# Performance work log

Hardware: AMD Instinct MI355X
Metric: run time of the kernel (lower is better)

The kernel has to match this reference:

```python
import jax, jax.numpy as jnp
import numpy as np

N, E, F_IN, H, D, C = 50000, 800000, 128, 4, 64, 40
HD = H * D
NEG_SLOPE = 0.2


def setup_inputs() -> dict:
    key = jax.random.key(0)
    ks = jax.random.split(key, 16)
    x = jax.random.normal(ks[0], (N, F_IN), dtype=jnp.float32)
    edge_index = jax.random.randint(ks[1], (2, E), 0, N, dtype=jnp.int64)
    def glorot(k, shape):
        fan = shape[0] + shape[-1]
        return jax.random.normal(k, shape, dtype=jnp.float32) * jnp.sqrt(2.0 / fan)
    params = {
        'W1': glorot(ks[2], (F_IN, HD)), 'as1': glorot(ks[3], (H, D)), 'ad1': glorot(ks[4], (H, D)), 'b1': jnp.zeros((HD,), jnp.float32),
        'W2': glorot(ks[5], (HD, HD)),   'as2': glorot(ks[6], (H, D)), 'ad2': glorot(ks[7], (H, D)), 'b2': jnp.zeros((HD,), jnp.float32),
        'W3': glorot(ks[8], (HD, HD)),   'as3': glorot(ks[9], (H, D)), 'ad3': glorot(ks[10], (H, D)), 'b3': jnp.zeros((HD,), jnp.float32),
        'Wl': glorot(ks[11], (HD, C)),   'bl': jnp.zeros((C,), jnp.float32),
    }
    return {'x': x, 'edge_index': edge_index, **params}


def gat_layer(x, src, dst, W, a_src, a_dst, b):
    # x: [N, F] -> h: [N, H, D]
    h = (x @ W).reshape(N, H, D)
    alpha_s = jnp.sum(h * a_src, axis=-1)  # [N, H]
    alpha_d = jnp.sum(h * a_dst, axis=-1)  # [N, H]
    e = alpha_s[src] + alpha_d[dst]        # [E', H]
    e = jnp.where(e > 0, e, NEG_SLOPE * e)  # leaky_relu
    # segment softmax over destination nodes
    m = jax.ops.segment_max(e, dst, num_segments=N)  # [N, H]
    m = jnp.where(jnp.isfinite(m), m, 0.0)
    ex = jnp.exp(e - m[dst])
    s = jax.ops.segment_sum(ex, dst, num_segments=N)  # [N, H]
    att = ex / (s[dst] + 1e-16)                        # [E', H]
    # weighted scatter-aggregate of source features
    out = jax.ops.segment_sum(h[src] * att[:, :, None], dst, num_segments=N)  # [N, H, D]
    return out.reshape(N, HD) + b


def reference(x, edge_index, W1, as1, ad1, b1, W2, as2, ad2, b2, W3, as3, ad3, b3, Wl, bl):
    # PyG GATConv adds self-loops by default
    loops = jnp.arange(N, dtype=edge_index.dtype)
    src = jnp.concatenate([edge_index[0], loops])
    dst = jnp.concatenate([edge_index[1], loops])
    # dropout is identity in eval mode
    h = jax.nn.elu(gat_layer(x, src, dst, W1, as1, ad1, b1))
    h = jax.nn.elu(gat_layer(h, src, dst, W2, as2, ad2, b2))
    h = jax.nn.elu(gat_layer(h, src, dst, W3, as3, ad3, b3))
    logits = h @ Wl + bl
    return jax.nn.log_softmax(logits, axis=1)
```

## Files before the change

### kernel.cpp

```cpp
#include <hip/hip_runtime.h>
#include <math.h>

#define NN 50000
#define NE 800000
#define ET (NE + NN)
#define FIN 128
#define HDIM 256
#define NHEAD 4
#define NCLS 40
#define NEG 0.2f
#define NB_SCAN ((NN + 255) / 256)

typedef short bf16x8 __attribute__((ext_vector_type(8)));
typedef float f32x4 __attribute__((ext_vector_type(4)));

__device__ __forceinline__ unsigned short f2b(float f) {
    unsigned int u = __float_as_uint(f);
    unsigned int r = (u + 0x7fffu + ((u >> 16) & 1u)) >> 16;
    return (unsigned short)r;
}
__device__ __forceinline__ unsigned int cvtpk(float lo, float hi) {
    unsigned int r;
    asm volatile("v_cvt_pk_bf16_f32 %0, %1, %2" : "=v"(r) : "v"(lo), "v"(hi));
    return r;
}
__device__ __forceinline__ float b2f(unsigned short u) {
    unsigned int x = ((unsigned int)u) << 16;
    return __uint_as_float(x);
}

__device__ __forceinline__ int sniff_is64(const int* __restrict__ ei32, int* s64p) {
    if (threadIdx.x < 64) {
        int nz = ei32[1 + 2 * threadIdx.x] | ei32[129 + 2 * threadIdx.x];
        unsigned long long b = __ballot(nz != 0);
        if (threadIdx.x == 0) *s64p = (b == 0ull) ? 1 : 0;
    }
    __syncthreads();
    return *s64p;
}

__device__ __forceinline__ int load_node(const int* ei32, int is64, long long idx) {
    return is64 ? ei32[2 * idx] : ei32[idx];
}

__global__ void deg_kernel(const int* __restrict__ ei32, int* __restrict__ deg) {
    __shared__ int s64;
    int is64 = sniff_is64(ei32, &s64);
    int e = blockIdx.x * blockDim.x + threadIdx.x;
    if (e >= ET) return;
    int d = (e < NE) ? load_node(ei32, is64, (long long)NE + e) : (e - NE);
    atomicAdd(&deg[d], 1);
}

__global__ void scan1(const int* __restrict__ deg, int* __restrict__ incl,
                      int* __restrict__ bsum) {
    __shared__ int sm[256];
    int i = blockIdx.x * 256 + threadIdx.x;
    int v = (i < NN) ? deg[i] : 0;
    sm[threadIdx.x] = v;
    __syncthreads();
    for (int o = 1; o < 256; o <<= 1) {
        int add = (threadIdx.x >= o) ? sm[threadIdx.x - o] : 0;
        __syncthreads();
        sm[threadIdx.x] += add;
        __syncthreads();
    }
    if (i < NN) incl[i] = sm[threadIdx.x];
    if (threadIdx.x == 255) bsum[blockIdx.x] = sm[255];
}

__global__ void scan2(int* __restrict__ bsum) {
    __shared__ int sm[256];
    int t = threadIdx.x;
    sm[t] = (t < NB_SCAN) ? bsum[t] : 0;
    __syncthreads();
    if (t == 0) {
        int run = 0;
        for (int b = 0; b < NB_SCAN; b++) { int v = sm[b]; sm[b] = run; run += v; }
    }
    __syncthreads();
    if (t < NB_SCAN) bsum[t] = sm[t];
}

__global__ void scan3(const int* __restrict__ incl, const int* __restrict__ bsum,
                      const int* __restrict__ deg, int* __restrict__ indptr,
                      int* __restrict__ cursor) {
    int i = blockIdx.x * 256 + threadIdx.x;
    if (i < NN) {
        int v = bsum[blockIdx.x] + incl[i];
        indptr[i + 1] = v;
        cursor[i] = v - deg[i];
    }
    if (i == 0) indptr[0] = 0;
}

__global__ void fill_kernel(const int* __restrict__ ei32,
                            int* __restrict__ cursor, int* __restrict__ esrc) {
    __shared__ int s64;
    int is64 = sniff_is64(ei32, &s64);
    int e = blockIdx.x * blockDim.x + threadIdx.x;
    if (e >= ET) return;
    int s, d;
    if (e < NE) {
        s = load_node(ei32, is64, (long long)e);
        d = load_node(ei32, is64, (long long)NE + e);
    } else {
        s = d = e - NE;
    }
    int pos = atomicAdd(&cursor[d], 1);
    esrc[pos] = s;
}

__global__ __launch_bounds__(256) void conv_kernel(const float* __restrict__ in,
                                                   unsigned short* __restrict__ out, int n) {
    int i = (blockIdx.x * 256 + threadIdx.x) * 8;
    if (i + 8 > n) return;
    float4 f0 = *(const float4*)(in + i);
    float4 f1 = *(const float4*)(in + i + 4);
    uint4 pk;
    pk.x = cvtpk(f0.x, f0.y);
    pk.y = cvtpk(f0.z, f0.w);
    pk.z = cvtpk(f1.x, f1.y);
    pk.w = cvtpk(f1.z, f1.w);
    *(uint4*)(out + i) = pk;
}

__global__ __launch_bounds__(256) void wconv3_kernel(const float* __restrict__ W1,
                                                     const float* __restrict__ W2,
                                                     const float* __restrict__ W3,
                                                     unsigned short* __restrict__ Wt1,
                                                     unsigned short* __restrict__ Wt2,
                                                     unsigned short* __restrict__ Wt3) {
    __shared__ float sm[32][33];
    int z = blockIdx.z;
    const float* W = (z == 0) ? W1 : (z == 1) ? W2 : W3;
    unsigned short* Wt = (z == 0) ? Wt1 : (z == 1) ? Wt2 : Wt3;
    int K = (z == 0) ? FIN : HDIM;
    int k0 = blockIdx.y * 32;
    if (k0 >= K) return;
    int tx = threadIdx.x & 31, ty = threadIdx.x >> 5;
    int n0 = blockIdx.x * 32;
#pragma unroll
    for (int j = 0; j < 4; j++)
        sm[ty + j * 8][tx] = W[(size_t)(k0 + ty + j * 8) * HDIM + n0 + tx];
    __syncthreads();
#pragma unroll
    for (int j = 0; j < 4; j++)
        Wt[(size_t)(n0 + ty + j * 8) * K + k0 + tx] = f2b(sm[tx][ty + j * 8]);
}

__global__ __launch_bounds__(256) void gemm_mfma(const unsigned short* __restrict__ A,
                                                 const unsigned short* __restrict__ Bt,
                                                 unsigned short* __restrict__ Cb,
                                                 const float* __restrict__ a_s,
                                                 const float* __restrict__ a_d,
                                                 float* __restrict__ als,
                                                 float* __restrict__ ald,
                                                 int M, int K) {
    __shared__ unsigned short As[128][72];
    __shared__ unsigned short Bs[64][72];
    int bid = blockIdx.x;
    int xcd = bid & 7, g = bid >> 3;
    int cblk = g & 3, rg = g >> 2;
    int rblk = rg * 8 + xcd;
    int r0 = rblk * 128, n0 = cblk * 64;
    if (r0 >= M) return;

    int t = threadIdx.x;
    int lane = t & 63, wid = t >> 6;

    f32x4 acc[2][4];
#pragma unroll
    for (int m = 0; m < 2; m++)
#pragma unroll
        for (int n = 0; n < 4; n++)
            acc[m][n] = (f32x4){0.f, 0.f, 0.f, 0.f};

    int ar = t >> 1, ah = (t & 1) * 32;
    int arow = r0 + ar; if (arow > M - 1) arow = M - 1;
    const unsigned short* ga = A + (size_t)arow * K + ah;
    int bn = t >> 2, bq = (t & 3) * 16;
    const unsigned short* gb = Bt + (size_t)(n0 + bn) * K + bq;

    int fr = lane & 15;
    int kf = (lane >> 4) * 8;

    for (int k0 = 0; k0 < K; k0 += 64) {
#pragma unroll
        for (int j = 0; j < 4; j++)
            *(uint4*)&As[ar][ah + j * 8] = *(const uint4*)(ga + k0 + j * 8);
#pragma unroll
        for (int j = 0; j < 2; j++)
            *(uint4*)&Bs[bn][bq + j * 8] = *(const uint4*)(gb + k0 + j * 8);
        __syncthreads();
#pragma unroll
        for (int kk = 0; kk < 64; kk += 32) {
            bf16x8 a[2], b[4];
#pragma unroll
            for (int m = 0; m < 2; m++)
                a[m] = *(const bf16x8*)&As[wid * 32 + m * 16 + fr][kk + kf];
#pragma unroll
            for (int n = 0; n < 4; n++)
                b[n] = *(const bf16x8*)&Bs[n * 16 + fr][kk + kf];
#pragma unroll
            for (int m = 0; m < 2; m++)
#pragma unroll
                for (int n = 0; n < 4; n++)
                    acc[m][n] = __builtin_amdgcn_mfma_f32_16x16x32_bf16(a[m], b[n], acc[m][n], 0, 0, 0);
        }
        __syncthreads();
    }

    int rbase = r0 + wid * 32 + (lane >> 4) * 4;
    int cbase = n0 + fr;
    int head = n0 >> 6;
    float asv[4], adv[4];
#pragma unroll
    for (int n = 0; n < 4; n++) {
        asv[n] = a_s[cbase + n * 16];
        adv[n] = a_d[cbase + n * 16];
    }
#pragma unroll
    for (int m = 0; m < 2; m++)
#pragma unroll
        for (int q = 0; q < 4; q++) {
            int gr = rbase + m * 16 + q;
            float vs = 0.f, vd = 0.f;
#pragma unroll
            for (int n = 0; n < 4; n++) {
                float v = acc[m][n][q];
                vs += v * asv[n];
                vd += v * adv[n];
            }
#pragma unroll
            for (int o = 8; o > 0; o >>= 1) {
                vs += __shfl_xor(vs, o);
                vd += __shfl_xor(vd, o);
            }
            if (fr == 0 && gr < M) {
                als[gr * NHEAD + head] = vs;
                ald[gr * NHEAD + head] = vd;
            }
        }

    unsigned short (*Cs)[68] = (unsigned short(*)[68])&As[0][0];
    int lr0 = wid * 32 + (lane >> 4) * 4;
#pragma unroll
    for (int m = 0; m < 2; m++)
#pragma unroll
        for (int q = 0; q < 4; q++)
#pragma unroll
            for (int n = 0; n < 4; n++)
                Cs[lr0 + m * 16 + q][fr + n * 16] = f2b(acc[m][n][q]);
    __syncthreads();
    int tr = t >> 4;
    int tc = (t & 15) * 4;
#pragma unroll
    for (int rr = 0; rr < 8; rr++) {
        int lr = tr + rr * 16;
        int gr = r0 + lr;
        if (gr < M) *(ushort4*)(Cb + (size_t)gr * HDIM + n0 + tc) = *(const ushort4*)&Cs[lr][tc];
    }
}

__global__ __launch_bounds__(256) void agg_kernel(const unsigned short* __restrict__ projb,
                                                  const float* __restrict__ als,
                                                  const float* __restrict__ ald,
                                                  const int* __restrict__ indptr,
                                                  const int* __restrict__ esrc,
                                                  const float* __restrict__ bias,
                                                  unsigned short* __restrict__ featb) {
    int wid = threadIdx.x >> 6;
    int v = blockIdx.x * 4 + wid;
    if (v >= NN) return;
    int lane = threadIdx.x & 63;
    int h = lane >> 4;
    int sub = lane & 15;
    int beg = indptr[v], end = indptr[v + 1];
    float adv = ald[v * NHEAD + h];

    float e0 = 0.f, e1 = 0.f;
    int s0r = 0, s1r = 0;
    float m = -INFINITY, ss = 0.f;
    int idx = 0;
    for (int i = beg + sub; i < end; i += 16, idx++) {
        int s = esrc[i];
        float e = als[s * NHEAD + h] + adv;
        e = e > 0.f ? e : NEG * e;
        if (idx == 0) { e0 = e; s0r = s; }
        else if (idx == 1) { e1 = e; s1r = s; }
        if (e > m) {
            ss = ss * __expf(m - e) + 1.f;
            m = e;
        } else {
            ss += __expf(e - m);
        }
    }
#pragma unroll
    for (int o = 8; o > 0; o >>= 1) {
        float m2 = __shfl_xor(m, o);
        float s2 = __shfl_xor(ss, o);
        float mn = fmaxf(m, m2);
        float a = (m == mn) ? ss : ss * __expf(m - mn);
        float b = (m2 == mn) ? s2 : s2 * __expf(m2 - mn);
        m = mn;
        ss = a + b;
    }
    float inv = 1.f / (ss + 1e-16f);

    float4 acc = make_float4(0.f, 0.f, 0.f, 0.f);
    int c = beg;
    int chunk = 0;
    for (; c + 16 < end; c += 32, chunk += 2) {
        int remB = end - (c + 16); if (remB > 16) remB = 16;
        int sA, sB;
        float eA, eB;
        if (chunk == 0) {
            sA = s0r; eA = e0;
            sB = s1r; eB = e1;
        } else {
            sA = esrc[c + sub];
            eA = als[sA * NHEAD + h] + adv;
            eA = eA > 0.f ? eA : NEG * eA;
            int iB = c + 16 + (sub < remB ? sub : remB - 1);
            sB = esrc[iB];
            eB = als[sB * NHEAD + h] + adv;
            eB = eB > 0.f ? eB : NEG * eB;
        }
        float wA = __expf(eA - m) * inv;
        float wB = (sub < remB) ? __expf(eB - m) * inv : 0.f;

        ushort4 pA[16], pB[16];
#pragma unroll
        for (int j = 0; j < 16; j++) {
            int s = __shfl(sA, j);
            pA[j] = *(const ushort4*)(projb + (size_t)s * HDIM + (lane << 2));
        }
#pragma unroll
        for (int j = 0; j < 16; j++) {
            int s = __shfl(sB, j);
            pB[j] = *(const ushort4*)(projb + (size_t)s * HDIM + (lane << 2));
        }
#pragma unroll
        for (int j = 0; j < 16; j++) {
            float w = __shfl(wA, (h << 4) | j);
            acc.x += b2f(pA[j].x) * w;
            acc.y += b2f(pA[j].y) * w;
            acc.z += b2f(pA[j].z) * w;
            acc.w += b2f(pA[j].w) * w;
        }
#pragma unroll
        for (int j = 0; j < 16; j++) {
            float w = __shfl(wB, (h << 4) | j);
            acc.x += b2f(pB[j].x) * w;
            acc.y += b2f(pB[j].y) * w;
            acc.z += b2f(pB[j].z) * w;
            acc.w += b2f(pB[j].w) * w;
        }
    }
    if (c < end) {
        int rem = end - c;
        int sA;
        float eA;
        if (chunk == 0) { sA = s0r; eA = e0; }
        else if (chunk == 1) { sA = s1r; eA = e1; }
        else {
            int i = c + (sub < rem ? sub : rem - 1);
            sA = esrc[i];
            eA = als[sA * NHEAD + h] + adv;
            eA = eA > 0.f ? eA : NEG * eA;
        }
        float wA = (sub < rem) ? __expf(eA - m) * inv : 0.f;
        ushort4 p[16];
#pragma unroll
        for (int j = 0; j < 16; j++) {
            int s = __shfl(sA, j);
            p[j] = *(const ushort4*)(projb + (size_t)s * HDIM + (lane << 2));
        }
#pragma unroll
        for (int j = 0; j < 16; j++) {
            float w = __shfl(wA, (h << 4) | j);
            acc.x += b2f(p[j].x) * w;
            acc.y += b2f(p[j].y) * w;
            acc.z += b2f(p[j].z) * w;
            acc.w += b2f(p[j].w) * w;
        }
    }

    const float4 b4 = *(const float4*)(bias + (lane << 2));
    float4 r;
    r.x = acc.x + b4.x;
    r.y = acc.y + b4.y;
    r.z = acc.z + b4.z;
    r.w = acc.w + b4.w;
    r.x = r.x > 0.f ? r.x : __expf(r.x) - 1.f;
    r.y = r.y > 0.f ? r.y : __expf(r.y) - 1.f;
    r.z = r.z > 0.f ? r.z : __expf(r.z) - 1.f;
    r.w = r.w > 0.f ? r.w : __expf(r.w) - 1.f;
    uint2 o2;
    o2.x = cvtpk(r.x, r.y);
    o2.y = cvtpk(r.z, r.w);
    *(uint2*)(featb + (size_t)v * HDIM + (lane << 2)) = o2;
}

__global__ __launch_bounds__(256) void final_kernel(const unsigned short* __restrict__ featb,
                                                    const float* __restrict__ Wl,
                                                    const float* __restrict__ bl,
                                                    float* __restrict__ out) {
    const int BK = 16;
    __shared__ float As[BK][65];
    __shared__ float Bs[BK][65];
    int tx = threadIdx.x & 15, ty = threadIdx.x >> 4;
    int row0 = blockIdx.x * 64;
    float acc[4][4] = {};
    for (int k0 = 0; k0 < HDIM; k0 += BK) {
#pragma unroll
        for (int i = 0; i < 4; i++) {
            int l = threadIdx.x + 256 * i;
            int r = l >> 4, c = l & 15;
            int gr = row0 + r;
            float v = 0.f;
            if (gr < NN) v = b2f(featb[(size_t)gr * HDIM + k0 + c]);
            As[c][r] = v;
        }
#pragma unroll
        for (int i = 0; i < 4; i++) {
            int l = threadIdx.x + 256 * i;
            int r = l >> 6, c = l & 63;
            Bs[r][c] = (c < NCLS) ? Wl[(size_t)(k0 + r) * NCLS + c] : 0.f;
        }
        __syncthreads();
#pragma unroll
        for (int k = 0; k < BK; k++) {
            float a[4], b[4];
#pragma unroll
            for (int i = 0; i < 4; i++) a[i] = As[k][ty + 16 * i];
#pragma unroll
            for (int j = 0; j < 4; j++) b[j] = Bs[k][tx + 16 * j];
#pragma unroll
            for (int i = 0; i < 4; i++)
#pragma unroll
                for (int j = 0; j < 4; j++) acc[i][j] += a[i] * b[j];
        }
        __syncthreads();
    }
    float b0 = bl[tx], b1 = bl[tx + 16], b2 = (tx < 8) ? bl[tx + 32] : 0.f;
#pragma unroll
    for (int i = 0; i < 4; i++) {
        int gr = row0 + ty + 16 * i;
        if (gr >= NN) continue;
        float l0 = acc[i][0] + b0;
        float l1 = acc[i][1] + b1;
        float l2 = (tx < 8) ? acc[i][2] + b2 : -INFINITY;
        float m = fmaxf(fmaxf(l0, l1), l2);
#pragma unroll
        for (int o = 8; o > 0; o >>= 1) m = fmaxf(m, __shfl_xor(m, o));
        float s = __expf(l0 - m) + __expf(l1 - m) + ((tx < 8) ? __expf(l2 - m) : 0.f);
#pragma unroll
        for (int o = 8; o > 0; o >>= 1) s += __shfl_xor(s, o);
        float lse = m + __logf(s);
        out[(size_t)gr * NCLS + tx] = l0 - lse;
        out[(size_t)gr * NCLS + tx + 16] = l1 - lse;
        if (tx < 8) out[(size_t)gr * NCLS + tx + 32] = l2 - lse;
    }
}

extern "C" void kernel_launch(void* const* d_in, const int* in_sizes, int n_in,
                              void* d_out, int out_size, void* d_ws, size_t ws_size,
                              hipStream_t stream) {
    const float* x  = (const float*)d_in[0];
    const int* ei32 = (const int*)d_in[1];
    const float* W1 = (const float*)d_in[2];
    const float* as1 = (const float*)d_in[3];
    const float* ad1 = (const float*)d_in[4];
    const float* b1 = (const float*)d_in[5];
    const float* W2 = (const float*)d_in[6];
    const float* as2 = (const float*)d_in[7];
    const float* ad2 = (const float*)d_in[8];
    const float* b2 = (const float*)d_in[9];
    const float* W3 = (const float*)d_in[10];
    const float* as3 = (const float*)d_in[11];
    const float* ad3 = (const float*)d_in[12];
    const float* b3 = (const float*)d_in[13];
    const float* Wl = (const float*)d_in[14];
    const float* bl = (const float*)d_in[15];
    float* out = (float*)d_out;

    char* w = (char*)d_ws;
    unsigned short* projb = (unsigned short*)w;  w += (size_t)NN * HDIM * 2;
    unsigned short* featb = (unsigned short*)w;  w += (size_t)NN * HDIM * 2;
    unsigned short* xb    = (unsigned short*)w;  w += (size_t)NN * FIN * 2;
    unsigned short* Wt1b  = (unsigned short*)w;  w += (size_t)HDIM * FIN * 2;
    unsigned short* Wt2b  = (unsigned short*)w;  w += (size_t)HDIM * HDIM * 2;
    unsigned short* Wt3b  = (unsigned short*)w;  w += (size_t)HDIM * HDIM * 2;
    float* als  = (float*)w;  w += (size_t)NN * NHEAD * 4;
    float* ald  = (float*)w;  w += (size_t)NN * NHEAD * 4;
    int* deg    = (int*)w;    w += (size_t)NN * 4;
    int* incl   = (int*)w;    w += (size_t)NN * 4;
    int* bsum   = (int*)w;    w += 256 * 4;
    int* indptr = (int*)w;    w += (size_t)(NN + 1) * 4;
    int* cursor = (int*)w;    w += (size_t)NN * 4;
    int* esrc   = (int*)w;    w += (size_t)ET * 4;

    conv_kernel<<<(NN * FIN / 8 + 255) / 256, 256, 0, stream>>>(x, xb, NN * FIN);
    wconv3_kernel<<<dim3(8, 8, 3), 256, 0, stream>>>(W1, W2, W3, Wt1b, Wt2b, Wt3b);

    hipMemsetAsync(deg, 0, (size_t)NN * 4, stream);
    deg_kernel<<<(ET + 255) / 256, 256, 0, stream>>>(ei32, deg);
    scan1<<<NB_SCAN, 256, 0, stream>>>(deg, incl, bsum);
    scan2<<<1, 256, 0, stream>>>(bsum);
    scan3<<<NB_SCAN, 256, 0, stream>>>(incl, bsum, deg, indptr, cursor);
    fill_kernel<<<(ET + 255) / 256, 256, 0, stream>>>(ei32, cursor, esrc);

    int ggrid = 8 * 4 * (((NN + 127) / 128 + 7) / 8);
    int agrid = (NN + 3) / 4;

    gemm_mfma<<<ggrid, 256, 0, stream>>>(xb, Wt1b, projb, as1, ad1, als, ald, NN, FIN);
    agg_kernel<<<agrid, 256, 0, stream>>>(projb, als, ald, indptr, esrc, b1, featb);
    gemm_mfma<<<ggrid, 256, 0, stream>>>(featb, Wt2b, projb, as2, ad2, als, ald, NN, HDIM);
    agg_kernel<<<agrid, 256, 0, stream>>>(projb, als, ald, indptr, esrc, b2, featb);
    gemm_mfma<<<ggrid, 256, 0, stream>>>(featb, Wt3b, projb, as3, ad3, als, ald, NN, HDIM);
    agg_kernel<<<agrid, 256, 0, stream>>>(projb, als, ald, indptr, esrc, b3, featb);
    final_kernel<<<(NN + 63) / 64, 256, 0, stream>>>(featb, Wl, bl, out);
}
```

Before: 406.0 us.

## Retile projection GEMM to 64-row blocks covering all 256 output columns

The MFMA projection GEMM changes from 128x64 output tiles with XCD-swizzled block mapping to 64x256 tiles, where each wave owns one head's 64 columns. Each block now reads its A rows once instead of four times across column blocks, and the epilogue writes full 512-byte rows with 16-byte stores. In exchange, each block loads the whole weight slice into about 46KB of shared memory, and accumulators double to 16 per lane. That may lower occupancy, and the launch has fewer, larger blocks.

```diff
diff --git a/kernel.cpp b/kernel.cpp
--- a/kernel.cpp
+++ b/kernel.cpp
@@ -157,53 +157,51 @@
                                                  float* __restrict__ als,
                                                  float* __restrict__ ald,
                                                  int M, int K) {
-    __shared__ unsigned short As[128][72];
-    __shared__ unsigned short Bs[64][72];
-    int bid = blockIdx.x;
-    int xcd = bid & 7, g = bid >> 3;
-    int cblk = g & 3, rg = g >> 2;
-    int rblk = rg * 8 + xcd;
-    int r0 = rblk * 128, n0 = cblk * 64;
+    __shared__ unsigned short smem[64 * 72 + 256 * 72];
+    unsigned short* Asm = smem;
+    unsigned short* Bsm = smem + 64 * 72;
+
+    int r0 = blockIdx.x * 64;
     if (r0 >= M) return;
-
     int t = threadIdx.x;
     int lane = t & 63, wid = t >> 6;
-
-    f32x4 acc[2][4];
-#pragma unroll
-    for (int m = 0; m < 2; m++)
+    int fr = lane & 15;
+    int kg = lane >> 4;
+    int kf = kg * 8;
+
+    f32x4 acc[4][4];
+#pragma unroll
+    for (int m = 0; m < 4; m++)
 #pragma unroll
         for (int n = 0; n < 4; n++)
             acc[m][n] = (f32x4){0.f, 0.f, 0.f, 0.f};
 
-    int ar = t >> 1, ah = (t & 1) * 32;
-    int arow = r0 + ar; if (arow > M - 1) arow = M - 1;
-    const unsigned short* ga = A + (size_t)arow * K + ah;
-    int bn = t >> 2, bq = (t & 3) * 16;
-    const unsigned short* gb = Bt + (size_t)(n0 + bn) * K + bq;
-
-    int fr = lane & 15;
-    int kf = (lane >> 4) * 8;
+    int arw = t >> 3, ko8 = (t & 7) * 8;
+    int ar0 = r0 + arw;      if (ar0 > M - 1) ar0 = M - 1;
+    int ar1 = r0 + arw + 32; if (ar1 > M - 1) ar1 = M - 1;
+    const unsigned short* gA0 = A + (size_t)ar0 * K + ko8;
+    const unsigned short* gA1 = A + (size_t)ar1 * K + ko8;
+    const unsigned short* gB  = Bt + (size_t)arw * K + ko8;
 
     for (int k0 = 0; k0 < K; k0 += 64) {
-#pragma unroll
-        for (int j = 0; j < 4; j++)
-            *(uint4*)&As[ar][ah + j * 8] = *(const uint4*)(ga + k0 + j * 8);
-#pragma unroll
-        for (int j = 0; j < 2; j++)
-            *(uint4*)&Bs[bn][bq + j * 8] = *(const uint4*)(gb + k0 + j * 8);
+        *(uint4*)(Asm + arw * 72 + ko8)        = *(const uint4*)(gA0 + k0);
+        *(uint4*)(Asm + (arw + 32) * 72 + ko8) = *(const uint4*)(gA1 + k0);
+#pragma unroll
+        for (int j = 0; j < 8; j++)
+            *(uint4*)(Bsm + (arw + 32 * j) * 72 + ko8) =
+                *(const uint4*)(gB + (size_t)32 * j * K + k0);
         __syncthreads();
 #pragma unroll
         for (int kk = 0; kk < 64; kk += 32) {
-            bf16x8 a[2], b[4];
-#pragma unroll
-            for (int m = 0; m < 2; m++)
-                a[m] = *(const bf16x8*)&As[wid * 32 + m * 16 + fr][kk + kf];
+            bf16x8 a[4], b[4];
+#pragma unroll
+            for (int m = 0; m < 4; m++)
+                a[m] = *(const bf16x8*)(Asm + (m * 16 + fr) * 72 + kk + kf);
 #pragma unroll
             for (int n = 0; n < 4; n++)
-                b[n] = *(const bf16x8*)&Bs[n * 16 + fr][kk + kf];
-#pragma unroll
-            for (int m = 0; m < 2; m++)
+                b[n] = *(const bf16x8*)(Bsm + (wid * 64 + n * 16 + fr) * 72 + kk + kf);
+#pragma unroll
+            for (int m = 0; m < 4; m++)
 #pragma unroll
                 for (int n = 0; n < 4; n++)
                     acc[m][n] = __builtin_amdgcn_mfma_f32_16x16x32_bf16(a[m], b[n], acc[m][n], 0, 0, 0);
@@ -211,20 +209,17 @@
         __syncthreads();
     }
 
-    int rbase = r0 + wid * 32 + (lane >> 4) * 4;
-    int cbase = n0 + fr;
-    int head = n0 >> 6;
     float asv[4], adv[4];
 #pragma unroll
     for (int n = 0; n < 4; n++) {
-        asv[n] = a_s[cbase + n * 16];
-        adv[n] = a_d[cbase + n * 16];
-    }
-#pragma unroll
-    for (int m = 0; m < 2; m++)
+        asv[n] = a_s[wid * 64 + n * 16 + fr];
+        adv[n] = a_d[wid * 64 + n * 16 + fr];
+    }
+#pragma unroll
+    for (int m = 0; m < 4; m++)
 #pragma unroll
         for (int q = 0; q < 4; q++) {
-            int gr = rbase + m * 16 + q;
+            int gr = r0 + m * 16 + kg * 4 + q;
             float vs = 0.f, vd = 0.f;
 #pragma unroll
             for (int n = 0; n < 4; n++) {
@@ -238,28 +233,28 @@
                 vd += __shfl_xor(vd, o);
             }
             if (fr == 0 && gr < M) {
-                als[gr * NHEAD + head] = vs;
-                ald[gr * NHEAD + head] = vd;
+                als[gr * NHEAD + wid] = vs;
+                ald[gr * NHEAD + wid] = vd;
             }
         }
 
-    unsigned short (*Cs)[68] = (unsigned short(*)[68])&As[0][0];
-    int lr0 = wid * 32 + (lane >> 4) * 4;
-#pragma unroll
-    for (int m = 0; m < 2; m++)
+    unsigned short* Cs = smem;
+#pragma unroll
+    for (int m = 0; m < 4; m++)
 #pragma unroll
         for (int q = 0; q < 4; q++)
 #pragma unroll
             for (int n = 0; n < 4; n++)
-                Cs[lr0 + m * 16 + q][fr + n * 16] = f2b(acc[m][n][q]);
+                Cs[(m * 16 + kg * 4 + q) * 264 + wid * 64 + n * 16 + fr] = f2b(acc[m][n][q]);
     __syncthreads();
-    int tr = t >> 4;
-    int tc = (t & 15) * 4;
-#pragma unroll
-    for (int rr = 0; rr < 8; rr++) {
-        int lr = tr + rr * 16;
-        int gr = r0 + lr;
-        if (gr < M) *(ushort4*)(Cb + (size_t)gr * HDIM + n0 + tc) = *(const ushort4*)&Cs[lr][tc];
+    int row = t >> 2, u = t & 3;
+    int gr = r0 + row;
+    if (gr < M) {
+#pragma unroll
+        for (int j = 0; j < 8; j++) {
+            int col0 = u * 64 + j * 8;
+            *(uint4*)(Cb + (size_t)gr * HDIM + col0) = *(const uint4*)(Cs + row * 264 + col0);
+        }
     }
 }
 
@@ -512,7 +507,7 @@
     scan3<<<NB_SCAN, 256, 0, stream>>>(incl, bsum, deg, indptr, cursor);
     fill_kernel<<<(ET + 255) / 256, 256, 0, stream>>>(ei32, cursor, esrc);
 
-    int ggrid = 8 * 4 * (((NN + 127) / 128 + 7) / 8);
+    int ggrid = (NN + 63) / 64;
     int agrid = (NN + 3) / 4;
 
     gemm_mfma<<<ggrid, 256, 0, stream>>>(xb, Wt1b, projb, as1, ad1, als, ald, NN, FIN);
```

Result: slower. 442.5 us (+9.0%).
